# Performance work log

Measured on AMD Instinct MI355X. Metric: run time of the kernel, lower is better.

Reference implementation:

```python
import jax, jax.numpy as jnp
import numpy as np

EPS = 1e-6


def setup_inputs() -> dict:
    key = jax.random.key(0)
    ks = jax.random.split(key, 7)
    T, B, D, n, r = 512, 32, 1024, 1024, 8
    x = jax.random.normal(ks[0], (T, B, D), dtype=jnp.float32)
    # xavier_uniform-like init for weights
    def xavier(k, shape):
        fan_in, fan_out = shape[1], shape[0]
        a = float(np.sqrt(6.0 / (fan_in + fan_out)))
        return jax.random.uniform(k, shape, dtype=jnp.float32, minval=-a, maxval=a)
    W_k = xavier(ks[1], (n, D))
    W_v = xavier(ks[2], (n, D))
    W_q = xavier(ks[3], (n, D))
    W_kr = xavier(ks[4], (r, n))
    U0 = jnp.zeros((B, n, r), dtype=jnp.float32)
    V0 = jax.random.normal(ks[5], (B, n, r), dtype=jnp.float32) * 0.01
    return {"x": x, "W_k": W_k, "W_v": W_v, "W_q": W_q, "W_kr": W_kr, "U0": U0, "V0": V0}


def reference(x, W_k, W_v, W_q, W_kr, U0, V0):
    # x: [T, B, D]; state S = U @ V^T with U,V: [B, n, r]
    k = jnp.einsum('tbd,nd->tbn', x, W_k)
    v = jnp.einsum('tbd,nd->tbn', x, W_v)
    q = jnp.einsum('tbd,nd->tbn', x, W_q)
    V = V0  # V is never updated in the recurrence

    def step(U, kvq):
        k_t, v_t, q_t = kvq  # each [B, n]
        k_norm = k_t / (jnp.linalg.norm(k_t, axis=-1, keepdims=True) + EPS)
        Vtk = jnp.einsum('bnr,bn->br', V, k_norm)
        retrieved = jnp.einsum('bnr,br->bn', U, Vtk)
        delta = v_t - retrieved
        k_r = k_norm @ W_kr.T  # [B, r]
        U_new = jnp.tanh(U + delta[:, :, None] * k_r[:, None, :])
        Vtq = jnp.einsum('bnr,bn->br', V, q_t)
        Sq = jnp.einsum('bnr,br->bn', U_new, Vtq)
        out = Sq * jax.nn.silu(Sq)
        return U_new, out

    U_final, output = jax.lax.scan(step, U0, (k, v, q))
    return output, (U_final, V)
```

## Files before the change

### kernel.cpp

```cpp
#include <hip/hip_runtime.h>
#include <hip/hip_bf16.h>

typedef __attribute__((ext_vector_type(8))) short short8;
typedef __attribute__((ext_vector_type(4))) short short4v;
typedef __attribute__((ext_vector_type(4))) float f32x4;
typedef unsigned short u16;

__device__ inline float b2f(u16 u) {
    unsigned int i = ((unsigned int)u) << 16;
    float f; __builtin_memcpy(&f, &i, 4); return f;
}
__device__ inline u16 f2b(float f) {
    unsigned int i; __builtin_memcpy(&i, &f, 4);
    unsigned int r = (i + 0x7FFFu + ((i >> 16) & 1u)) >> 16;
    return (u16)r;
}

__device__ inline float xsum32(float x) {
    unsigned u; __builtin_memcpy(&u, &x, 4);
    auto r = __builtin_amdgcn_permlane32_swap(u, u, false, false);
    unsigned s0 = r[0], s1 = r[1];
    float f0, f1; __builtin_memcpy(&f0, &s0, 4); __builtin_memcpy(&f1, &s1, 4);
    return f0 + f1;
}

#define GLDS(g, l) __builtin_amdgcn_global_load_lds( \
    (const __attribute__((address_space(1))) void*)(g), \
    (__attribute__((address_space(3))) void*)(l), 16, 0, 0)

__global__ __launch_bounds__(256) void cvt_k(const float* __restrict__ src,
                                             u16* __restrict__ dst, int n4)
{
    const int i = blockIdx.x * blockDim.x + threadIdx.x;
    if (i < n4) {
        const f32x4 v = ((const f32x4*)src)[i];
        short4v o;
        o.x = (short)f2b(v.x); o.y = (short)f2b(v.y);
        o.z = (short)f2b(v.z); o.w = (short)f2b(v.w);
        ((short4v*)dst)[i] = o;
    }
}

__global__ __launch_bounds__(256) void vT_k(const float* __restrict__ V0,
                                            float* __restrict__ V0T)
{
    const int gid = blockIdx.x * 256 + threadIdx.x;
    const int b = gid >> 9, j = (gid >> 6) & 7, n0 = (gid & 63) * 16;
    const float* src = V0 + (long)b * 8192 + (long)n0 * 8 + j;
    float* dst = V0T + (long)b * 8192 + (long)j * 1024 + n0;
#pragma unroll
    for (int i = 0; i < 16; i += 4) {
        f32x4 o = { src[(i + 0) * 8], src[(i + 1) * 8],
                    src[(i + 2) * 8], src[(i + 3) * 8] };
        *(f32x4*)(dst + i) = o;
    }
}

__global__ __launch_bounds__(256) void gemm_kvq(
    const u16* __restrict__ X, const u16* __restrict__ Wbf,
    u16* __restrict__ Ko, u16* __restrict__ Vo, u16* __restrict__ Qo)
{
    __shared__ u16 As[128 * 64];
    __shared__ u16 Bs[128 * 64];

    const int bm = blockIdx.x;
    const int bn = blockIdx.y;
    const int widx = bn >> 3;
    const int n0 = (bn & 7) * 128;
    const u16* W = Wbf + (long)widx * 1048576;
    u16* O = (widx == 0) ? Ko : (widx == 1 ? Vo : Qo);

    const int tid = threadIdx.x;
    const int wave = tid >> 6;
    const int lane = tid & 63;

    const int srow = lane >> 3;
    const int scol = ((lane & 7) ^ srow) * 8;

    const int wm = (wave & 1) * 64;
    const int wn = (wave >> 1) * 64;
    const int qd = lane >> 4;
    const int ln = lane & 15;
    const int lx = ln & 7;

    f32x4 acc[4][4];
#pragma unroll
    for (int i = 0; i < 4; i++)
#pragma unroll
        for (int j = 0; j < 4; j++) acc[i][j] = (f32x4){0.f, 0.f, 0.f, 0.f};

    for (int k0 = 0; k0 < 1024; k0 += 64) {
        __syncthreads();
#pragma unroll
        for (int c = 0; c < 4; c++) {
            const int chunk = wave * 4 + c;
            const int row = chunk * 8 + srow;
            const u16* ga = X + (long)(bm * 128 + row) * 1024 + k0 + scol;
            GLDS(ga, &As[chunk * 512]);
            const u16* gb = W + (long)(n0 + row) * 1024 + k0 + scol;
            GLDS(gb, &Bs[chunk * 512]);
        }
        __syncthreads();
#pragma unroll
        for (int kk = 0; kk < 2; kk++) {
            short8 af[4], bf[4];
#pragma unroll
            for (int mt = 0; mt < 4; mt++)
                af[mt] = *(const short8*)&As[(wm + mt * 16 + ln) * 64 +
                                             (((kk * 4 + qd) ^ lx) * 8)];
#pragma unroll
            for (int nt = 0; nt < 4; nt++)
                bf[nt] = *(const short8*)&Bs[(wn + nt * 16 + ln) * 64 +
                                             (((kk * 4 + qd) ^ lx) * 8)];
#pragma unroll
            for (int mt = 0; mt < 4; mt++)
#pragma unroll
                for (int nt = 0; nt < 4; nt++)
                    acc[mt][nt] = __builtin_amdgcn_mfma_f32_16x16x32_bf16(
                        af[mt], bf[nt], acc[mt][nt], 0, 0, 0);
        }
    }

#pragma unroll
    for (int mt = 0; mt < 4; mt++) {
#pragma unroll
        for (int nt = 0; nt < 4; nt++) {
            const int r0 = bm * 128 + wm + mt * 16 + qd * 4;
            const int c = n0 + wn + nt * 16 + ln;
#pragma unroll
            for (int r = 0; r < 4; r++)
                O[(long)(r0 + r) * 1024 + c] = f2b(acc[mt][nt][r]);
        }
    }
}

__global__ __launch_bounds__(256) void scal_k(
    const u16* __restrict__ K, const u16* __restrict__ Q,
    const float* __restrict__ V0T, const float* __restrict__ Wkr,
    float* __restrict__ S)
{
    const int b  = blockIdx.x & 31;
    const int t0 = (blockIdx.x >> 5) * 4;
    const int tid = threadIdx.x;
    const int j = tid & 7, c = tid >> 3;
    const int n0 = c * 32;

    f32x4 vv[8], ww[8];
    {
        const f32x4* vp = (const f32x4*)(V0T + (long)b * 8192 + (long)j * 1024 + n0);
        const f32x4* wp = (const f32x4*)(Wkr + (long)j * 1024 + n0);
#pragma unroll
        for (int i = 0; i < 8; i++) { vv[i] = vp[i]; ww[i] = wp[i]; }
    }

    float avk[4], akr[4], avq[4], ass[4];
#pragma unroll
    for (int dt = 0; dt < 4; dt++) { avk[dt] = akr[dt] = avq[dt] = ass[dt] = 0.f; }

#pragma unroll
    for (int dt = 0; dt < 4; dt++) {
        const long m = (long)(t0 + dt) * 32 + b;
        const short8* kp = (const short8*)(K + m * 1024 + n0);
        const short8* qp = (const short8*)(Q + m * 1024 + n0);
#pragma unroll
        for (int i = 0; i < 4; i++) {
            const short8 kb = kp[i], qb = qp[i];
#pragma unroll
            for (int e = 0; e < 8; e++) {
                const int idx = i * 8 + e;
                const float kv = b2f((u16)kb[e]);
                const float qv = b2f((u16)qb[e]);
                const float vj = vv[idx >> 2][idx & 3];
                const float wj = ww[idx >> 2][idx & 3];
                avk[dt] = fmaf(vj, kv, avk[dt]);
                akr[dt] = fmaf(wj, kv, akr[dt]);
                avq[dt] = fmaf(vj, qv, avq[dt]);
                ass[dt] = fmaf(kv, kv, ass[dt]);
            }
        }
    }

    __shared__ float red[4][4][3][8];
    __shared__ float ssr[4][4];
    const int wave = tid >> 6, lane = tid & 63;
#pragma unroll
    for (int dt = 0; dt < 4; dt++) {
        float a = avk[dt], k2 = akr[dt], q = avq[dt], s = ass[dt];
#pragma unroll
        for (int off = 8; off < 64; off <<= 1) {
            a  += __shfl_xor(a,  off, 64);
            k2 += __shfl_xor(k2, off, 64);
            q  += __shfl_xor(q,  off, 64);
            s  += __shfl_xor(s,  off, 64);
        }
        if (lane < 8) {
            red[wave][dt][0][lane] = a;
            red[wave][dt][1][lane] = k2;
            red[wave][dt][2][lane] = q;
        }
        if (lane == 0) ssr[wave][dt] = s;
    }
    __syncthreads();
    if (tid < 128) {
        const int dt = tid >> 5, rr = tid & 31;
        if (rr < 24) {
            const int v = rr >> 3, jj = rr & 7;
            float s = red[0][dt][v][jj] + red[1][dt][v][jj] +
                      red[2][dt][v][jj] + red[3][dt][v][jj];
            if (v != 2) {
                const float n2 = ssr[0][dt] + ssr[1][dt] + ssr[2][dt] + ssr[3][dt];
                const float inv = 1.0f / (sqrtf(n2) + 1e-6f);
                s *= (v == 0) ? (0.5f * inv) : (2.0f * inv);
            } else {
                s *= 0.5f;
            }
            S[((long)b * 512 + t0 + dt) * 32 + v * 8 + jj] = s;
        }
    }
}

__global__ __launch_bounds__(128) void scan_k(
    const u16* __restrict__ Vbuf, const float* __restrict__ S,
    const float* __restrict__ U0, float* __restrict__ outp,
    float* __restrict__ Ufin)
{
    __shared__ float Sl[512 * 32];

    const int b = blockIdx.x >> 4;
    const int chunk = blockIdx.x & 15;
    const int wave = threadIdx.x >> 6, lane = threadIdx.x & 63;
    const int rh = lane >> 5;
    const int n = chunk * 64 + wave * 32 + (lane & 31);
    const int so = rh * 4;

    {
        const f32x4* Sg = (const f32x4*)(S + (long)b * 16384);
        f32x4* Sd = (f32x4*)Sl;
        for (int i = threadIdx.x; i < 4096; i += 128) Sd[i] = Sg[i];
    }

    float U[4];
    {
        const float* u0 = U0 + ((long)b * 1024 + n) * 8 + so;
#pragma unroll
        for (int j2 = 0; j2 < 4; j2++) U[j2] = 2.0f * u0[j2];
    }

    const u16* vp0 = Vbuf + (long)b * 1024 + n;
    u16 vnx[16];
#pragma unroll
    for (int i = 0; i < 16; i++) vnx[i] = vp0[(long)i * 32768];

    __syncthreads();

    f32x4 sc[3], sn[3];
#pragma unroll
    for (int r = 0; r < 3; r++) sc[r] = *(const f32x4*)&Sl[r * 8 + so];
#pragma unroll
    for (int r = 0; r < 3; r++) sn[r] = *(const f32x4*)&Sl[32 + r * 8 + so];

    float* op = outp + (long)b * 1024 + n;

    for (int t0 = 0; t0 < 512; t0 += 16) {
        float vcur[16];
#pragma unroll
        for (int i = 0; i < 16; i++) vcur[i] = b2f(vnx[i]);
        const int tn = (t0 + 16 < 512) ? (t0 + 16) : t0;
#pragma unroll
        for (int i = 0; i < 16; i++) vnx[i] = vp0[(long)(tn + i) * 32768];

#pragma unroll
        for (int i = 0; i < 16; i++) {
            const int t = t0 + i;
            const int tf = (t + 2 < 512) ? (t + 2) : t;
            f32x4 sm[3];
#pragma unroll
            for (int r = 0; r < 3; r++) sm[r] = *(const f32x4*)&Sl[tf * 32 + r * 8 + so];

            const f32x4 a = sc[0], Kk = sc[1], Qq = sc[2];
#pragma unroll
            for (int r = 0; r < 3; r++) { sc[r] = sn[r]; sn[r] = sm[r]; }

            float pr = fmaf(U[0], a.x, U[1] * a.y) + fmaf(U[2], a.z, U[3] * a.w);
            const float ret = xsum32(pr);
            const float delta = vcur[i] - ret;

            const float kr4[4] = {Kk.x, Kk.y, Kk.z, Kk.w};
            const float vq4[4] = {Qq.x, Qq.y, Qq.z, Qq.w};

            float sq0 = 0.f, sq1 = 0.f;
#pragma unroll
            for (int j2 = 0; j2 < 4; j2++) {
                const float xx = fmaf(delta, kr4[j2], U[j2]);
                const float e = __expf(xx);
                const float rc = __builtin_amdgcn_rcpf(e + 1.0f);
                const float u = fmaf(-4.0f, rc, 2.0f);
                U[j2] = u;
                if (j2 & 1) sq1 = fmaf(u, vq4[j2], sq1);
                else        sq0 = fmaf(u, vq4[j2], sq0);
            }
            const float Sq = xsum32(sq0 + sq1);
            const float sg = __builtin_amdgcn_rcpf(1.0f + __expf(-Sq));
            const float o = Sq * Sq * sg;
            if (rh == 0) op[(long)t * 32768] = o;
        }
    }

    *(f32x4*)(Ufin + ((long)b * 1024 + n) * 8 + so) =
        (f32x4){0.5f * U[0], 0.5f * U[1], 0.5f * U[2], 0.5f * U[3]};
}

__global__ __launch_bounds__(256) void vcopy_k(const float* __restrict__ src,
                                               float* __restrict__ dst)
{
    const int i = blockIdx.x * blockDim.x + threadIdx.x;
    ((f32x4*)dst)[i] = ((const f32x4*)src)[i];
}

extern "C" void kernel_launch(void* const* d_in, const int* in_sizes, int n_in,
                              void* d_out, int out_size, void* d_ws, size_t ws_size,
                              hipStream_t stream)
{
    const float* x   = (const float*)d_in[0];
    const float* Wk  = (const float*)d_in[1];
    const float* Wv  = (const float*)d_in[2];
    const float* Wq  = (const float*)d_in[3];
    const float* Wkr = (const float*)d_in[4];
    const float* U0  = (const float*)d_in[5];
    const float* V0  = (const float*)d_in[6];
    float* out = (float*)d_out;

    char* ws = (char*)d_ws;
    u16*   Xbf = (u16*)(ws);
    u16*   Wbf = (u16*)(ws + 33554432);
    u16*   Kb  = (u16*)(ws + 39845888);
    u16*   Vb  = (u16*)(ws + 73400320);
    u16*   Qb  = (u16*)(ws + 106954752);
    float* Sc  = (float*)(ws + 140509184);
    float* V0T = (float*)(ws + 142606336);

    cvt_k<<<16384, 256, 0, stream>>>(x,  Xbf,               4194304);
    cvt_k<<<1024,  256, 0, stream>>>(Wk, Wbf,                262144);
    cvt_k<<<1024,  256, 0, stream>>>(Wv, Wbf + 1048576,      262144);
    cvt_k<<<1024,  256, 0, stream>>>(Wq, Wbf + 2097152,      262144);
    vT_k <<<64,    256, 0, stream>>>(V0, V0T);

    gemm_kvq<<<dim3(128, 24), 256, 0, stream>>>(Xbf, Wbf, Kb, Vb, Qb);
    scal_k  <<<4096, 256, 0, stream>>>(Kb, Qb, V0T, Wkr, Sc);
    scan_k  <<<512, 128, 0, stream>>>(Vb, Sc, U0, out, out + 16777216);
    vcopy_k <<<256, 256, 0, stream>>>(V0, out + 17039360);
}
```

Measured before the change: 408.6 us.

## Rewrite KVQ GEMM as 256x256 tile with 4-stage LDS pipeline

Replaces the 128x128 single-buffered bf16 GEMM with a 256x256-tile, 512-thread kernel that uses a 4-deep ring of 32 KB LDS stages fed by global_load_lds. Loads for future k-steps are issued between MFMA halves, with manual vmcnt waits and s_setprio around the MFMA bursts. A block-index swizzle groups tiles for L2 reuse. This aims to hide global-load latency and raise arithmetic intensity, at the cost of 128 KB LDS per block (one block per CU) and more complex hand-tuned synchronization.

```diff
diff --git a/kernel.cpp b/kernel.cpp
--- a/kernel.cpp
+++ b/kernel.cpp
@@ -27,6 +27,10 @@
 #define GLDS(g, l) __builtin_amdgcn_global_load_lds( \
     (const __attribute__((address_space(1))) void*)(g), \
     (__attribute__((address_space(3))) void*)(l), 16, 0, 0)
+
+#define KWAIT(N) asm volatile("s_waitcnt lgkmcnt(0)\n\t" \
+                              "s_waitcnt vmcnt(" #N ")\n\t" \
+                              "s_barrier" ::: "memory")
 
 __global__ __launch_bounds__(256) void cvt_k(const float* __restrict__ src,
                                              u16* __restrict__ dst, int n4)
@@ -56,80 +60,121 @@
     }
 }
 
-__global__ __launch_bounds__(256) void gemm_kvq(
-    const u16* __restrict__ X, const u16* __restrict__ Wbf,
+__global__ __launch_bounds__(512) void gemm256_kvq(
+    const u16* __restrict__ Xbf, const u16* __restrict__ Wbf,
     u16* __restrict__ Ko, u16* __restrict__ Vo, u16* __restrict__ Qo)
 {
-    __shared__ u16 As[128 * 64];
-    __shared__ u16 Bs[128 * 64];
-
-    const int bm = blockIdx.x;
-    const int bn = blockIdx.y;
-    const int widx = bn >> 3;
-    const int n0 = (bn & 7) * 128;
-    const u16* W = Wbf + (long)widx * 1048576;
+    __shared__ u16 lds[65536];
+
+    const int bid = blockIdx.x;
+    const int swz = (bid & 7) * 96 + (bid >> 3);
+    const int bm = swz / 12, bnx = swz % 12;
+    const int widx = bnx >> 2;
+    const int nbase = (bnx & 3) * 256;
+    const int m0 = bm * 256;
+    const u16* Wp = Wbf + (long)widx * 1048576;
     u16* O = (widx == 0) ? Ko : (widx == 1 ? Vo : Qo);
 
     const int tid = threadIdx.x;
-    const int wave = tid >> 6;
+    const int w = tid >> 6;
     const int lane = tid & 63;
-
-    const int srow = lane >> 3;
-    const int scol = ((lane & 7) ^ srow) * 8;
-
-    const int wm = (wave & 1) * 64;
-    const int wn = (wave >> 1) * 64;
-    const int qd = lane >> 4;
-    const int ln = lane & 15;
-    const int lx = ln & 7;
-
-    f32x4 acc[4][4];
-#pragma unroll
-    for (int i = 0; i < 4; i++)
-#pragma unroll
-        for (int j = 0; j < 4; j++) acc[i][j] = (f32x4){0.f, 0.f, 0.f, 0.f};
-
-    for (int k0 = 0; k0 < 1024; k0 += 64) {
-        __syncthreads();
-#pragma unroll
-        for (int c = 0; c < 4; c++) {
-            const int chunk = wave * 4 + c;
-            const int row = chunk * 8 + srow;
-            const u16* ga = X + (long)(bm * 128 + row) * 1024 + k0 + scol;
-            GLDS(ga, &As[chunk * 512]);
-            const u16* gb = W + (long)(n0 + row) * 1024 + k0 + scol;
-            GLDS(gb, &Bs[chunk * 512]);
-        }
-        __syncthreads();
-#pragma unroll
-        for (int kk = 0; kk < 2; kk++) {
-            short8 af[4], bf[4];
-#pragma unroll
-            for (int mt = 0; mt < 4; mt++)
-                af[mt] = *(const short8*)&As[(wm + mt * 16 + ln) * 64 +
-                                             (((kk * 4 + qd) ^ lx) * 8)];
-#pragma unroll
-            for (int nt = 0; nt < 4; nt++)
-                bf[nt] = *(const short8*)&Bs[(wn + nt * 16 + ln) * 64 +
-                                             (((kk * 4 + qd) ^ lx) * 8)];
-#pragma unroll
-            for (int mt = 0; mt < 4; mt++)
-#pragma unroll
-                for (int nt = 0; nt < 4; nt++)
-                    acc[mt][nt] = __builtin_amdgcn_mfma_f32_16x16x32_bf16(
-                        af[mt], bf[nt], acc[mt][nt], 0, 0, 0);
-        }
-    }
-
-#pragma unroll
-    for (int mt = 0; mt < 4; mt++) {
-#pragma unroll
-        for (int nt = 0; nt < 4; nt++) {
-            const int r0 = bm * 128 + wm + mt * 16 + qd * 4;
-            const int c = n0 + wn + nt * 16 + ln;
-#pragma unroll
-            for (int r = 0; r < 4; r++)
-                O[(long)(r0 + r) * 1024 + c] = f2b(acc[mt][nt][r]);
+    const int wm = (w >> 2) * 128;
+    const int wn = (w & 3) * 64;
+    const int ln = lane & 15, qd = lane >> 4;
+
+    const int q8 = lane >> 3, s8 = lane & 7;
+    const int cc = s8 ^ q8;
+    const u16* p0; const u16* p1; const u16* p2; const u16* p3;
+    {
+        auto mk = [&](int l) -> const u16* {
+            const int r = l * 64 + w * 8 + q8;
+            return (cc < 4)
+                ? (Xbf + (long)(m0 + r) * 1024 + cc * 8)
+                : (Wp  + (long)(nbase + r) * 1024 + (cc - 4) * 8);
+        };
+        p0 = mk(0); p1 = mk(1); p2 = mk(2); p3 = mk(3);
+    }
+
+    int aoff[8], boff[4];
+#pragma unroll
+    for (int mf = 0; mf < 8; ++mf) {
+        const int ro = wm + mf * 16 + ln;
+        aoff[mf] = ro * 128 + ((qd ^ (ro & 7)) * 16);
+    }
+#pragma unroll
+    for (int nf = 0; nf < 4; ++nf) {
+        const int rb = wn + nf * 16 + ln;
+        boff[nf] = rb * 128 + (((4 + qd) ^ (rb & 7)) * 16);
+    }
+
+    f32x4 acc[8][4];
+#pragma unroll
+    for (int i = 0; i < 8; ++i)
+#pragma unroll
+        for (int j = 0; j < 4; ++j) acc[i][j] = (f32x4){0.f, 0.f, 0.f, 0.f};
+
+#pragma unroll
+    for (int tt = 0; tt < 3; ++tt) {
+        char* db = (char*)lds + tt * 32768 + w * 1024;
+        GLDS(p0, db);
+        GLDS(p1, db + 8192);
+        GLDS(p2, db + 16384);
+        GLDS(p3, db + 24576);
+        p0 += 32; p1 += 32; p2 += 32; p3 += 32;
+    }
+    KWAIT(8);
+
+    for (int t = 0; t < 32; ++t) {
+        const char* bb = (const char*)lds + (t & 3) * 32768;
+        short8 a[8], bfr[4];
+#pragma unroll
+        for (int mf = 0; mf < 4; ++mf) a[mf] = *(const short8*)(bb + aoff[mf]);
+#pragma unroll
+        for (int nf = 0; nf < 4; ++nf) bfr[nf] = *(const short8*)(bb + boff[nf]);
+        if (t < 29) {
+            char* db = (char*)lds + ((t + 3) & 3) * 32768 + w * 1024;
+            GLDS(p0, db);
+            GLDS(p1, db + 8192);
+            p0 += 32; p1 += 32;
+        }
+        __builtin_amdgcn_s_setprio(1);
+#pragma unroll
+        for (int mf = 0; mf < 4; ++mf)
+#pragma unroll
+            for (int nf = 0; nf < 4; ++nf)
+                acc[mf][nf] = __builtin_amdgcn_mfma_f32_16x16x32_bf16(
+                    a[mf], bfr[nf], acc[mf][nf], 0, 0, 0);
+        __builtin_amdgcn_s_setprio(0);
+#pragma unroll
+        for (int mf = 4; mf < 8; ++mf) a[mf] = *(const short8*)(bb + aoff[mf]);
+        if (t < 29) {
+            char* db = (char*)lds + ((t + 3) & 3) * 32768 + w * 1024;
+            GLDS(p2, db + 16384);
+            GLDS(p3, db + 24576);
+            p2 += 32; p3 += 32;
+        }
+        __builtin_amdgcn_s_setprio(1);
+#pragma unroll
+        for (int mf = 4; mf < 8; ++mf)
+#pragma unroll
+            for (int nf = 0; nf < 4; ++nf)
+                acc[mf][nf] = __builtin_amdgcn_mfma_f32_16x16x32_bf16(
+                    a[mf], bfr[nf], acc[mf][nf], 0, 0, 0);
+        __builtin_amdgcn_s_setprio(0);
+        if (t < 29)       KWAIT(8);
+        else if (t == 29) KWAIT(4);
+        else if (t == 30) KWAIT(0);
+    }
+
+#pragma unroll
+    for (int mf = 0; mf < 8; ++mf) {
+#pragma unroll
+        for (int nf = 0; nf < 4; ++nf) {
+            const int r0 = m0 + wm + mf * 16 + qd * 4;
+            const int c  = nbase + wn + nf * 16 + ln;
+#pragma unroll
+            for (int r = 0; r < 4; ++r)
+                O[(long)(r0 + r) * 1024 + c] = f2b(acc[mf][nf][r]);
         }
     }
 }
@@ -345,7 +390,7 @@
     cvt_k<<<1024,  256, 0, stream>>>(Wq, Wbf + 2097152,      262144);
     vT_k <<<64,    256, 0, stream>>>(V0, V0T);
 
-    gemm_kvq<<<dim3(128, 24), 256, 0, stream>>>(Xbf, Wbf, Kb, Vb, Qb);
+    gemm256_kvq<<<768, 512, 0, stream>>>(Xbf, Wbf, Kb, Vb, Qb);
     scal_k  <<<4096, 256, 0, stream>>>(Kb, Qb, V0T, Wkr, Sc);
     scan_k  <<<512, 128, 0, stream>>>(Vb, Sc, U0, out, out + 16777216);
     vcopy_k <<<256, 256, 0, stream>>>(V0, out + 17039360);
```

Result: no change. 409.2 us (+0.2%).
